# Kernel optimization log

Hardware: AMD Instinct MI355X
Metric: run time of the kernel (lower is better)

Reference implementation:

```python
import jax, jax.numpy as jnp
import numpy as np

NUM_CLASSES = 5
TEMPERATURE = 3.0
BATCH = 4_194_304


def setup_inputs() -> dict:
    key = jax.random.key(0)
    k1, k2 = jax.random.split(key)
    quality_score = jax.random.uniform(k1, (BATCH,), dtype=jnp.float32)
    class_logits = jax.random.normal(k2, (BATCH, NUM_CLASSES), dtype=jnp.float32)
    return {"quality_score": quality_score, "class_logits": class_logits}


def _soft_targets(score, num_classes):
    # Vectorized version of the per-sample python loop in the torch module.
    C = num_classes
    # int(clamp(score*C, 0, C-1)) -> floor for non-negative scores
    idx = jnp.floor(jnp.clip(score * C, 0.0, C - 1)).astype(jnp.int32)
    center = (idx.astype(score.dtype) + 0.5) / C
    dist = jnp.abs(score - center) * C
    cond_lo = (idx > 0) & (score < center)          # spill to class idx-1
    cond_hi = (idx < C - 1) & (score > center)      # spill to class idx+1
    has_nb = cond_lo | cond_hi
    main_val = jnp.where(has_nb, 1.0 - dist, 1.0)
    nb_idx = idx - cond_lo.astype(jnp.int32) + cond_hi.astype(jnp.int32)
    nb_val = jnp.where(has_nb, dist, 0.0)
    cols = jnp.arange(C)
    # [B, C] dense soft targets built by broadcasted one-hot masks (no scatter)
    soft = (main_val[:, None] * (cols[None, :] == idx[:, None])
            + nb_val[:, None] * (cols[None, :] == nb_idx[:, None]))
    return soft


def reference(quality_score, class_logits):
    T = TEMPERATURE
    C = class_logits.shape[-1]
    B = class_logits.shape[0]
    soft = _soft_targets(quality_score, C)
    p = jax.nn.softmax(soft / T, axis=-1)               # targets (probs)
    logq = jax.nn.log_softmax(class_logits / T, axis=-1)
    # F.kl_div(logq, p, reduction='batchmean') = sum p*(log p - logq) / B
    kl = jnp.sum(p * (jnp.log(p) - logq)) / B
    return kl * T * T
```

## Files before the change

kernel.cpp:

```cpp
#include <hip/hip_runtime.h>
#include <math.h>


constexpr int   kC     = 5;
constexpr float kInvT  = 1.0f / 3.0f;
constexpr float kExp13 = 1.3956124250860895f;
constexpr int   kBatch = 4194304;

__global__ void zero_out_kernel(float* out) {
    if (threadIdx.x == 0) out[0] = 0.0f;
}

__global__ __launch_bounds__(256) void kl_partial_kernel(
    const float* __restrict__ score,
    const float* __restrict__ logits,
    float* __restrict__ out) {

    const int q = blockIdx.x * blockDim.x + threadIdx.x;

    const float4 s4 = reinterpret_cast<const float4*>(score)[q];
    const float4* lrow = reinterpret_cast<const float4*>(logits + (size_t)q * 20);
    const float4 L0 = lrow[0], L1 = lrow[1], L2 = lrow[2], L3 = lrow[3], L4 = lrow[4];

    const float v[20] = {L0.x, L0.y, L0.z, L0.w,
                         L1.x, L1.y, L1.z, L1.w,
                         L2.x, L2.y, L2.z, L2.w,
                         L3.x, L3.y, L3.z, L3.w,
                         L4.x, L4.y, L4.z, L4.w};
    const float ss[4] = {s4.x, s4.y, s4.z, s4.w};

    float acc = 0.0f;
    #pragma unroll
    for (int r = 0; r < 4; ++r) {
        const float s  = ss[r];
        const float l0 = v[r * 5 + 0], l1 = v[r * 5 + 1], l2 = v[r * 5 + 2],
                    l3 = v[r * 5 + 3], l4 = v[r * 5 + 4];

        const float sc     = fminf(fmaxf(s * 5.0f, 0.0f), 4.0f);
        const int   idx    = (int)sc;
        const float center = ((float)idx + 0.5f) * 0.2f;
        float       d      = fabsf(s - center) * 5.0f;
        const bool  lo     = (idx > 0) && (s < center);
        const bool  hi     = (idx < kC - 1) && (s > center);
        const bool  nb     = lo || hi;
        d = nb ? d : 0.0f;
        const int nbi = idx + (hi ? 1 : 0) - (lo ? 1 : 0);

        const float e_nb   = __expf(d * kInvT);
        const float e_main = kExp13 * __builtin_amdgcn_rcpf(e_nb);

        const float S = l0 + l1 + l2 + l3 + l4;
        const float l_main = (idx == 0) ? l0 : (idx == 1) ? l1 :
                             (idx == 2) ? l2 : (idx == 3) ? l3 : l4;
        const float l_nb   = (nbi == 0) ? l0 : (nbi == 1) ? l1 :
                             (nbi == 2) ? l2 : (nbi == 3) ? l3 : l4;

        const float Zq = __expf(l0 * kInvT) + __expf(l1 * kInvT) +
                         __expf(l2 * kInvT) + __expf(l3 * kInvT) +
                         __expf(l4 * kInvT);

        const float Zp  = e_main + e_nb + 3.0f;
        const float rZp = __builtin_amdgcn_rcpf(Zp);
        const float Spa = e_main * (1.0f - d) + e_nb * d;
        const float Spl = e_main * l_main + e_nb * l_nb + (S - l_main - l_nb);

        acc += kInvT * (Spa - Spl) * rZp + __logf(Zq * rZp);
    }

    #pragma unroll
    for (int off = 32; off > 0; off >>= 1) acc += __shfl_down(acc, off, 64);

    __shared__ float wsum[4];
    const int lane = threadIdx.x & 63;
    const int wave = threadIdx.x >> 6;
    if (lane == 0) wsum[wave] = acc;
    __syncthreads();
    if (threadIdx.x == 0) {
        const float b = wsum[0] + wsum[1] + wsum[2] + wsum[3];
        atomicAdd(out, b * (9.0f / (float)kBatch));
    }
}

extern "C" void kernel_launch(void* const* d_in, const int* in_sizes, int n_in,
                              void* d_out, int out_size, void* d_ws, size_t ws_size,
                              hipStream_t stream) {
    const float* score  = (const float*)d_in[0];
    const float* logits = (const float*)d_in[1];
    float* out = (float*)d_out;

    const int B = in_sizes[0];
    const int nquads = B / 4;
    const int blocks = nquads / 256;

    zero_out_kernel<<<1, 64, 0, stream>>>(out);
    kl_partial_kernel<<<blocks, 256, 0, stream>>>(score, logits, out);
}
```

Before: 163.8 us.

## Stage logits tile in LDS with coalesced loads and two-pass reduction

Each block now loads a 512-quad tile of logits into shared memory using fully coalesced float4 loads, and each thread processes two quads read from LDS. This replaces the strided 80-byte-per-thread global reads. The per-block atomicAdd and the zero-init kernel are replaced by per-block partial sums in the workspace plus a single-block final reduction kernel. Shared-memory use grows to 40KB per block, which may limit occupancy, and the final kernel hardcodes 2048 partials.

```diff
diff --git a/kernel.cpp b/kernel.cpp
--- a/kernel.cpp
+++ b/kernel.cpp
@@ -7,26 +7,18 @@
 constexpr float kExp13 = 1.3956124250860895f;
 constexpr int   kBatch = 4194304;
 
-__global__ void zero_out_kernel(float* out) {
-    if (threadIdx.x == 0) out[0] = 0.0f;
-}
+constexpr int kThreads      = 256;
+constexpr int kQuadsPerTile = 512;
+constexpr int kTileVec4     = kQuadsPerTile * 5;
+constexpr int kBlocks       = (kBatch / 4) / kQuadsPerTile;
 
-__global__ __launch_bounds__(256) void kl_partial_kernel(
-    const float* __restrict__ score,
-    const float* __restrict__ logits,
-    float* __restrict__ out) {
-
-    const int q = blockIdx.x * blockDim.x + threadIdx.x;
-
-    const float4 s4 = reinterpret_cast<const float4*>(score)[q];
-    const float4* lrow = reinterpret_cast<const float4*>(logits + (size_t)q * 20);
-    const float4 L0 = lrow[0], L1 = lrow[1], L2 = lrow[2], L3 = lrow[3], L4 = lrow[4];
-
-    const float v[20] = {L0.x, L0.y, L0.z, L0.w,
-                         L1.x, L1.y, L1.z, L1.w,
-                         L2.x, L2.y, L2.z, L2.w,
-                         L3.x, L3.y, L3.z, L3.w,
-                         L4.x, L4.y, L4.z, L4.w};
+__device__ __forceinline__ float kl_quad(float4 P0, float4 P1, float4 P2,
+                                         float4 P3, float4 P4, float4 s4) {
+    const float v[20] = {P0.x, P0.y, P0.z, P0.w,
+                         P1.x, P1.y, P1.z, P1.w,
+                         P2.x, P2.y, P2.z, P2.w,
+                         P3.x, P3.y, P3.z, P3.w,
+                         P4.x, P4.y, P4.z, P4.w};
     const float ss[4] = {s4.x, s4.y, s4.z, s4.w};
 
     float acc = 0.0f;
@@ -66,18 +58,65 @@
 
         acc += kInvT * (Spa - Spl) * rZp + __logf(Zq * rZp);
     }
+    return acc;
+}
+
+__global__ __launch_bounds__(kThreads) void kl_partial_kernel(
+    const float* __restrict__ score,
+    const float* __restrict__ logits,
+    float* __restrict__ partial) {
+
+    __shared__ float4 slog4[kTileVec4];
+
+    const int t = threadIdx.x;
+    const int tile_quad0 = blockIdx.x * kQuadsPerTile;
+
+    const float4* gsrc = reinterpret_cast<const float4*>(logits + (size_t)tile_quad0 * 20);
+    #pragma unroll
+    for (int j = 0; j < 10; ++j) {
+        const int idx = t + kThreads * j;
+        slog4[idx] = gsrc[idx];
+    }
+
+    const float4* gsc = reinterpret_cast<const float4*>(score + (size_t)tile_quad0 * 4);
+    const float4 sA = gsc[t];
+    const float4 sB = gsc[t + kThreads];
+
+    __syncthreads();
+
+    const int a0 = t * 5, b0 = (t + kThreads) * 5;
+    float acc = kl_quad(slog4[a0], slog4[a0 + 1], slog4[a0 + 2], slog4[a0 + 3], slog4[a0 + 4], sA)
+              + kl_quad(slog4[b0], slog4[b0 + 1], slog4[b0 + 2], slog4[b0 + 3], slog4[b0 + 4], sB);
 
     #pragma unroll
     for (int off = 32; off > 0; off >>= 1) acc += __shfl_down(acc, off, 64);
 
     __shared__ float wsum[4];
-    const int lane = threadIdx.x & 63;
-    const int wave = threadIdx.x >> 6;
+    const int lane = t & 63;
+    const int wave = t >> 6;
     if (lane == 0) wsum[wave] = acc;
     __syncthreads();
-    if (threadIdx.x == 0) {
-        const float b = wsum[0] + wsum[1] + wsum[2] + wsum[3];
-        atomicAdd(out, b * (9.0f / (float)kBatch));
+    if (t == 0) {
+        partial[blockIdx.x] = wsum[0] + wsum[1] + wsum[2] + wsum[3];
+    }
+}
+
+__global__ __launch_bounds__(256) void kl_final_kernel(
+    const float* __restrict__ partial,
+    float* __restrict__ out) {
+    const int t = threadIdx.x;
+    const float4* p4 = reinterpret_cast<const float4*>(partial);
+    const float4 a = p4[t], b = p4[t + 256];
+    float acc = a.x + a.y + a.z + a.w + b.x + b.y + b.z + b.w;
+
+    #pragma unroll
+    for (int off = 32; off > 0; off >>= 1) acc += __shfl_down(acc, off, 64);
+
+    __shared__ float wsum[4];
+    if ((t & 63) == 0) wsum[t >> 6] = acc;
+    __syncthreads();
+    if (t == 0) {
+        out[0] = (wsum[0] + wsum[1] + wsum[2] + wsum[3]) * (9.0f / (float)kBatch);
     }
 }
 
@@ -86,12 +125,9 @@
                               hipStream_t stream) {
     const float* score  = (const float*)d_in[0];
     const float* logits = (const float*)d_in[1];
-    float* out = (float*)d_out;
+    float* out     = (float*)d_out;
+    float* partial = (float*)d_ws;
 
-    const int B = in_sizes[0];
-    const int nquads = B / 4;
-    const int blocks = nquads / 256;
-
-    zero_out_kernel<<<1, 64, 0, stream>>>(out);
-    kl_partial_kernel<<<blocks, 256, 0, stream>>>(score, logits, out);
+    kl_partial_kernel<<<kBlocks, kThreads, 0, stream>>>(score, logits, partial);
+    kl_final_kernel<<<1, 256, 0, stream>>>(partial, out);
 }
```

Result: faster. 135.9 us (-17.0%).
